# Kernel optimization log

Measured on AMD Instinct MI355X. Metric: run time of the kernel, lower is better.

The kernel has to match this reference:

```python
import jax, jax.numpy as jnp
import numpy as np

IN_CH = 32
H = W = 512
NUM_CAMS = 4096
N_RAYS = 524288
HIDDEN = 128
ALPHA = 1e-4
# tensor_config = ['xy','xz','yz'] -> axis index pairs into t (x,y,z)
AXES = ((0, 1), (0, 2), (1, 2))


def grid_sample_border(plane, coords):
    """Bilinear grid_sample, padding_mode='border', align_corners=True.
    plane: (C,H,W); coords: (N,2) in [-1,1], coords[:,0]->W axis, coords[:,1]->H axis.
    Returns (N,C)."""
    C, Hh, Ww = plane.shape
    x = (coords[:, 0] + 1.0) * 0.5 * (Ww - 1)
    y = (coords[:, 1] + 1.0) * 0.5 * (Hh - 1)
    x0f = jnp.floor(x)
    y0f = jnp.floor(y)
    wx = (x - x0f)[None, :]
    wy = (y - y0f)[None, :]
    x0 = jnp.clip(x0f.astype(jnp.int32), 0, Ww - 1)
    x1 = jnp.clip(x0f.astype(jnp.int32) + 1, 0, Ww - 1)
    y0 = jnp.clip(y0f.astype(jnp.int32), 0, Hh - 1)
    y1 = jnp.clip(y0f.astype(jnp.int32) + 1, 0, Hh - 1)
    v00 = plane[:, y0, x0]  # (C,N)
    v01 = plane[:, y0, x1]
    v10 = plane[:, y1, x0]
    v11 = plane[:, y1, x1]
    out = (v00 * (1 - wx) * (1 - wy) + v01 * wx * (1 - wy)
           + v10 * (1 - wx) * wy + v11 * wx * wy)
    return out.T


def exp_so3(r):
    """Rodrigues: axis-angle (N,3) -> rotation matrices (N,3,3)."""
    theta = jnp.linalg.norm(r, axis=-1)[:, None, None]
    z = jnp.zeros_like(r[:, 0])
    K = jnp.stack([z, -r[:, 2], r[:, 1],
                   r[:, 2], z, -r[:, 0],
                   -r[:, 1], r[:, 0], z], axis=-1).reshape(-1, 3, 3)
    A = jnp.sin(theta) / (theta + 1e-10)
    B = (1.0 - jnp.cos(theta)) / (theta * theta + 1e-10)
    return jnp.eye(3, dtype=r.dtype) + A * K + B * (K @ K)


def setup_inputs() -> dict:
    key = jax.random.key(0)
    ks = jax.random.split(key, 12)
    cam_id = jax.random.randint(ks[0], (N_RAYS,), 0, NUM_CAMS, dtype=jnp.int32)
    t = jax.random.uniform(ks[1], (NUM_CAMS, 3), minval=-1.0, maxval=1.0, dtype=jnp.float32)
    plane_xy = jax.random.normal(ks[2], (IN_CH, H, W), dtype=jnp.float32)
    plane_xz = jax.random.normal(ks[3], (IN_CH, H, W), dtype=jnp.float32)
    plane_yz = jax.random.normal(ks[4], (IN_CH, H, W), dtype=jnp.float32)
    in_chs = IN_CH * 3
    # kaiming_normal_ init: std = sqrt(2/fan_in)
    w1 = jax.random.normal(ks[5], (in_chs, HIDDEN), dtype=jnp.float32) * np.sqrt(2.0 / in_chs)
    b1 = jax.random.normal(ks[6], (HIDDEN,), dtype=jnp.float32) * 0.01
    w2 = jax.random.normal(ks[7], (HIDDEN, HIDDEN), dtype=jnp.float32) * np.sqrt(2.0 / HIDDEN)
    b2 = jax.random.normal(ks[8], (HIDDEN,), dtype=jnp.float32) * 0.01
    w3 = jax.random.normal(ks[9], (HIDDEN, 3), dtype=jnp.float32) * np.sqrt(2.0 / HIDDEN)
    b3 = jax.random.normal(ks[10], (3,), dtype=jnp.float32) * 0.01
    top = jax.random.normal(ks[11], (NUM_CAMS, 3, 4), dtype=jnp.float32)
    bottom = jnp.tile(jnp.array([[[0.0, 0.0, 0.0, 1.0]]], dtype=jnp.float32), (NUM_CAMS, 1, 1))
    init_c2w = jnp.concatenate([top, bottom], axis=1)  # (NUM_CAMS,4,4)
    return {"cam_id": cam_id, "t": t, "plane_xy": plane_xy, "plane_xz": plane_xz,
            "plane_yz": plane_yz, "w1": w1, "b1": b1, "w2": w2, "b2": b2,
            "w3": w3, "b3": b3, "init_c2w": init_c2w}


def reference(cam_id, t, plane_xy, plane_xz, plane_yz, w1, b1, w2, b2, w3, b3, init_c2w):
    ts = t[cam_id]  # (N,3) per-ray translation
    coords_all = jax.lax.stop_gradient(ts)  # coords use t.data in the original
    codes = []
    for plane, (ax, ay) in zip((plane_xy, plane_xz, plane_yz), AXES):
        coords = jnp.stack([coords_all[:, ax], coords_all[:, ay]], axis=-1)
        codes.append(grid_sample_border(plane, coords))  # (N,IN_CH)
    codes = jnp.concatenate(codes, axis=-1)  # (N, 3*IN_CH)
    h = jax.nn.silu(codes @ w1 + b1)
    h = jax.nn.silu(h @ w2 + b2)
    rot = (h @ w3 + b3) * ALPHA  # (N,3) axis-angle
    R = exp_so3(rot)  # (N,3,3)
    c2w34 = jnp.concatenate([R, ts[:, :, None]], axis=-1)  # (N,3,4)
    bottom = jnp.broadcast_to(jnp.array([0.0, 0.0, 0.0, 1.0], dtype=c2w34.dtype),
                              (c2w34.shape[0], 1, 4))
    c2ws = jnp.concatenate([c2w34, bottom], axis=1)  # (N,4,4)
    return c2ws @ init_c2w[cam_id]
```

## Files before the change

### kernel.cpp

```cpp
#include <hip/hip_runtime.h>
#include <hip/hip_bf16.h>
#include <math.h>

#define HWDIM 512
#define HIDDEN 128
#define N_RAYS 524288
#define NUM_CAMS 4096
#define ALPHA 1e-4f

typedef __attribute__((ext_vector_type(4))) float f32x4;
typedef __attribute__((ext_vector_type(8))) short bf16x8;

__device__ __forceinline__ unsigned short f2bf(float f) {
    union { float f; unsigned u; } v; v.f = f;
    unsigned r = v.u + 0x7FFFu + ((v.u >> 16) & 1u);
    return (unsigned short)(r >> 16);
}
__device__ __forceinline__ float bf2f(unsigned short s) {
    union { unsigned u; float f; } v; v.u = ((unsigned)s) << 16;
    return v.f;
}

__global__ __launch_bounds__(256) void sample_kernel(
    const float* __restrict__ t,
    const float* __restrict__ pxy,
    const float* __restrict__ pxz,
    const float* __restrict__ pyz,
    unsigned short* __restrict__ codes)
{
    const int g = blockIdx.x * 256 + threadIdx.x;
    const int cam = g / 192;
    const int r = g - cam * 192;
    const int f = r >> 1;
    const int ysel = r & 1;
    const int p = f >> 5;
    const int c = f & 31;

    const float ts0 = t[cam * 3 + 0];
    const float ts1 = t[cam * 3 + 1];
    const float ts2 = t[cam * 3 + 2];

    const float* plane;
    float cx, cy;
    if (p == 0)      { plane = pxy; cx = ts0; cy = ts1; }
    else if (p == 1) { plane = pxz; cx = ts0; cy = ts2; }
    else             { plane = pyz; cx = ts1; cy = ts2; }

    const float x = (cx + 1.0f) * 0.5f * (float)(HWDIM - 1);
    const float y = (cy + 1.0f) * 0.5f * (float)(HWDIM - 1);
    const float x0f = floorf(x);
    const float y0f = floorf(y);
    const float wx = x - x0f;
    const float wy = y - y0f;
    const int x0 = min(max((int)x0f, 0), HWDIM - 1);
    const int x1 = min(max((int)x0f + 1, 0), HWDIM - 1);
    const int y0 = min(max((int)y0f, 0), HWDIM - 1);
    const int y1 = min(max((int)y0f + 1, 0), HWDIM - 1);

    const int yr = ysel ? y1 : y0;
    const float wyv = ysel ? wy : (1.0f - wy);

    const float* base = plane + (size_t)c * (HWDIM * HWDIM) + yr * HWDIM;
    const float v0 = base[x0];
    const float v1 = base[x1];

    const float row = (v0 * (1.0f - wx) + v1 * wx) * wyv;
    const float other = __shfl_xor(row, 1);
    if (!ysel) codes[cam * 96 + f] = f2bf(row + other);
}

#define W1S 104
#define W2S 136
#define HS  136

__global__ __launch_bounds__(256) void mlp_kernel(
    const unsigned short* __restrict__ codes,
    const float* __restrict__ t,
    const float* __restrict__ w1, const float* __restrict__ b1,
    const float* __restrict__ w2, const float* __restrict__ b2,
    const float* __restrict__ w3, const float* __restrict__ b3,
    const float* __restrict__ init_c2w,
    float* __restrict__ table)
{
    const int tid  = threadIdx.x;
    const int lane = tid & 63;
    const int wave = tid >> 6;
    const int cam0 = blockIdx.x * 16;
    const int ncol = lane & 15;
    const int kgrp = lane >> 4;

    __shared__ unsigned short w1t[128][W1S];
    __shared__ unsigned short w2t[128][W2S];
    __shared__ unsigned short h1t[16][HS];
    __shared__ unsigned short h2t[16][HS];
    __shared__ float b1s[128], b2s[128], w3s[384];
    __shared__ float rotc[16][3];
    __shared__ float c2ws[16][12];

    {
        const float4* w1v = (const float4*)w1;
        for (int i = tid; i < (96 * 128) / 4; i += 256) {
            const float4 v = w1v[i];
            const int flat = i * 4;
            const int k = flat >> 7, n = flat & 127;
            w1t[n + 0][k] = f2bf(v.x);
            w1t[n + 1][k] = f2bf(v.y);
            w1t[n + 2][k] = f2bf(v.z);
            w1t[n + 3][k] = f2bf(v.w);
        }
        const float4* w2v = (const float4*)w2;
        for (int i = tid; i < (128 * 128) / 4; i += 256) {
            const float4 v = w2v[i];
            const int flat = i * 4;
            const int k = flat >> 7, n = flat & 127;
            w2t[n + 0][k] = f2bf(v.x);
            w2t[n + 1][k] = f2bf(v.y);
            w2t[n + 2][k] = f2bf(v.z);
            w2t[n + 3][k] = f2bf(v.w);
        }
    }
    if (tid < 128) { b1s[tid] = b1[tid]; b2s[tid] = b2[tid]; }
    for (int i = tid; i < 384; i += 256) w3s[i] = w3[i];
    __syncthreads();

    const int nb0 = wave * 32 + ncol;
    const int nb1 = nb0 + 16;

    f32x4 acc0, acc1;
    {
        const float bv0 = b1s[nb0], bv1 = b1s[nb1];
        acc0 = (f32x4){bv0, bv0, bv0, bv0};
        acc1 = (f32x4){bv1, bv1, bv1, bv1};
    }
    const unsigned short* arow = codes + (size_t)(cam0 + ncol) * 96;
    #pragma unroll
    for (int k0 = 0; k0 < 96; k0 += 32) {
        const bf16x8 a   = *reinterpret_cast<const bf16x8*>(arow + k0 + kgrp * 8);
        const bf16x8 bb0 = *reinterpret_cast<const bf16x8*>(&w1t[nb0][k0 + kgrp * 8]);
        const bf16x8 bb1 = *reinterpret_cast<const bf16x8*>(&w1t[nb1][k0 + kgrp * 8]);
        acc0 = __builtin_amdgcn_mfma_f32_16x16x32_bf16(a, bb0, acc0, 0, 0, 0);
        acc1 = __builtin_amdgcn_mfma_f32_16x16x32_bf16(a, bb1, acc1, 0, 0, 0);
    }
    #pragma unroll
    for (int r = 0; r < 4; ++r) {
        const int camr = kgrp * 4 + r;
        const float v0 = acc0[r];
        const float v1 = acc1[r];
        h1t[camr][nb0] = f2bf(v0 / (1.0f + __expf(-v0)));
        h1t[camr][nb1] = f2bf(v1 / (1.0f + __expf(-v1)));
    }
    __syncthreads();

    {
        const float bv0 = b2s[nb0], bv1 = b2s[nb1];
        acc0 = (f32x4){bv0, bv0, bv0, bv0};
        acc1 = (f32x4){bv1, bv1, bv1, bv1};
    }
    #pragma unroll
    for (int k0 = 0; k0 < 128; k0 += 32) {
        const bf16x8 a   = *reinterpret_cast<const bf16x8*>(&h1t[ncol][k0 + kgrp * 8]);
        const bf16x8 bb0 = *reinterpret_cast<const bf16x8*>(&w2t[nb0][k0 + kgrp * 8]);
        const bf16x8 bb1 = *reinterpret_cast<const bf16x8*>(&w2t[nb1][k0 + kgrp * 8]);
        acc0 = __builtin_amdgcn_mfma_f32_16x16x32_bf16(a, bb0, acc0, 0, 0, 0);
        acc1 = __builtin_amdgcn_mfma_f32_16x16x32_bf16(a, bb1, acc1, 0, 0, 0);
    }
    #pragma unroll
    for (int r = 0; r < 4; ++r) {
        const int camr = kgrp * 4 + r;
        const float v0 = acc0[r];
        const float v1 = acc1[r];
        h2t[camr][nb0] = f2bf(v0 / (1.0f + __expf(-v0)));
        h2t[camr][nb1] = f2bf(v1 / (1.0f + __expf(-v1)));
    }
    __syncthreads();

    if (tid < 64) {
        const int cam = tid >> 2, c = tid & 3;
        if (c < 3) {
            float acc = b3[c];
            for (int k = 0; k < 128; ++k)
                acc += bf2f(h2t[cam][k]) * w3s[k * 3 + c];
            rotc[cam][c] = acc * ALPHA;
        }
    }
    __syncthreads();

    if (tid < 16) {
        const int cam = tid;
        const float a = rotc[cam][0], b = rotc[cam][1], c = rotc[cam][2];
        const float th2 = a * a + b * b + c * c;
        const float th = sqrtf(th2);
        const float A = sinf(th) / (th + 1e-10f);
        const float B = (1.0f - cosf(th)) / (th2 + 1e-10f);
        const float ts0 = t[(cam0 + cam) * 3 + 0];
        const float ts1 = t[(cam0 + cam) * 3 + 1];
        const float ts2 = t[(cam0 + cam) * 3 + 2];
        c2ws[cam][0]  = 1.0f + B * (-(c * c + b * b));
        c2ws[cam][1]  = A * (-c) + B * (a * b);
        c2ws[cam][2]  = A * b + B * (a * c);
        c2ws[cam][3]  = ts0;
        c2ws[cam][4]  = A * c + B * (a * b);
        c2ws[cam][5]  = 1.0f + B * (-(c * c + a * a));
        c2ws[cam][6]  = A * (-a) + B * (b * c);
        c2ws[cam][7]  = ts1;
        c2ws[cam][8]  = A * (-b) + B * (a * c);
        c2ws[cam][9]  = A * a + B * (b * c);
        c2ws[cam][10] = 1.0f + B * (-(a * a + b * b));
        c2ws[cam][11] = ts2;
    }
    __syncthreads();

    {
        const int cam = tid >> 4, e = tid & 15, i = e >> 2, j = e & 3;
        const float* ic = init_c2w + (size_t)(cam0 + cam) * 16;
        float v;
        if (i < 3) {
            const float* cw = c2ws[cam];
            v = cw[i * 4 + 0] * ic[0 + j]
              + cw[i * 4 + 1] * ic[4 + j]
              + cw[i * 4 + 2] * ic[8 + j]
              + cw[i * 4 + 3] * ic[12 + j];
        } else {
            v = ic[12 + j];
        }
        table[(size_t)cam0 * 16 + tid] = v;
    }
}

__global__ __launch_bounds__(256) void gather_kernel(
    const int* __restrict__ cam_id,
    const float4* __restrict__ table,
    float4* __restrict__ out)
{
    const int idx = blockIdx.x * blockDim.x + threadIdx.x;
    if (idx >= N_RAYS * 4) return;
    const int ray = idx >> 2;
    const int q = idx & 3;
    const int cid = cam_id[ray];
    out[idx] = table[cid * 4 + q];
}

extern "C" void kernel_launch(void* const* d_in, const int* in_sizes, int n_in,
                              void* d_out, int out_size, void* d_ws, size_t ws_size,
                              hipStream_t stream) {
    const int*   cam_id   = (const int*)  d_in[0];
    const float* t        = (const float*)d_in[1];
    const float* pxy      = (const float*)d_in[2];
    const float* pxz      = (const float*)d_in[3];
    const float* pyz      = (const float*)d_in[4];
    const float* w1       = (const float*)d_in[5];
    const float* b1       = (const float*)d_in[6];
    const float* w2       = (const float*)d_in[7];
    const float* b2       = (const float*)d_in[8];
    const float* w3       = (const float*)d_in[9];
    const float* b3       = (const float*)d_in[10];
    const float* init_c2w = (const float*)d_in[11];

    float* table = (float*)d_ws;
    unsigned short* codes = (unsigned short*)((char*)d_ws + NUM_CAMS * 16 * 4);

    sample_kernel<<<(NUM_CAMS * 192) / 256, 256, 0, stream>>>(t, pxy, pxz, pyz, codes);

    mlp_kernel<<<NUM_CAMS / 16, 256, 0, stream>>>(
        codes, t, w1, b1, w2, b2, w3, b3, init_c2w, table);

    const int total = N_RAYS * 4;
    gather_kernel<<<(total + 255) / 256, 256, 0, stream>>>(
        cam_id, (const float4*)table, (float4*)d_out);
}
```

Baseline: 43.76 us.

## Bin cameras by plane row and sample rows cooperatively from LDS

Replaces the per-camera scattered bilinear gathers with a three-stage pipeline. Cameras are first binned by (plane, row) with atomics, then one block per row stages all 32 channels of that row into LDS as bf16, and each block serves the bilinear taps for every camera in its bin. The MLP kernel now sums the two row partials and packs them into an LDS A-tile. This swaps random gathers for coalesced row streaming, but every block reads a full row whether or not any camera falls in it, so each call streams all three planes. It also adds two extra launches, rounds plane values to bf16 before interpolation, and silently drops cameras if a bin exceeds BINCAP.

```diff
diff --git a/kernel.cpp b/kernel.cpp
--- a/kernel.cpp
+++ b/kernel.cpp
@@ -7,6 +7,7 @@
 #define N_RAYS 524288
 #define NUM_CAMS 4096
 #define ALPHA 1e-4f
+#define BINCAP 64
 
 typedef __attribute__((ext_vector_type(4))) float f32x4;
 typedef __attribute__((ext_vector_type(8))) short bf16x8;
@@ -21,52 +22,104 @@
     return v.f;
 }
 
-__global__ __launch_bounds__(256) void sample_kernel(
+__global__ __launch_bounds__(256) void zero_kernel(unsigned int* __restrict__ cnt) {
+    const int i = blockIdx.x * 256 + threadIdx.x;
+    if (i < 3 * HWDIM) cnt[i] = 0u;
+}
+
+__global__ __launch_bounds__(256) void bin_build(
     const float* __restrict__ t,
+    unsigned int* __restrict__ cnt,
+    uint4* __restrict__ bins)
+{
+    const int cam = blockIdx.x * 256 + threadIdx.x;
+    const float ts0 = t[cam * 3 + 0];
+    const float ts1 = t[cam * 3 + 1];
+    const float ts2 = t[cam * 3 + 2];
+
+    #pragma unroll
+    for (int p = 0; p < 3; ++p) {
+        const float cx = (p == 2) ? ts1 : ts0;
+        const float cy = (p == 0) ? ts1 : ts2;
+        const float x = (cx + 1.0f) * 0.5f * (float)(HWDIM - 1);
+        const float y = (cy + 1.0f) * 0.5f * (float)(HWDIM - 1);
+        const float x0f = floorf(x);
+        const float y0f = floorf(y);
+        const float wx = x - x0f;
+        const float wy = y - y0f;
+        const int x0 = min(max((int)x0f, 0), HWDIM - 1);
+        const int x1 = min(max((int)x0f + 1, 0), HWDIM - 1);
+        const int y0 = min(max((int)y0f, 0), HWDIM - 1);
+        const int y1 = min(max((int)y0f + 1, 0), HWDIM - 1);
+
+        #pragma unroll
+        for (int ysel = 0; ysel < 2; ++ysel) {
+            const int row = ysel ? y1 : y0;
+            const float wv = ysel ? wy : (1.0f - wy);
+            const int bin = p * HWDIM + row;
+            const unsigned slot = atomicAdd(&cnt[bin], 1u);
+            if (slot < BINCAP) {
+                uint4 e;
+                e.x = (unsigned)cam | ((unsigned)ysel << 12)
+                    | ((unsigned)x0 << 13) | ((unsigned)x1 << 22);
+                e.y = __float_as_uint(wx);
+                e.z = __float_as_uint(wv);
+                e.w = 0u;
+                bins[bin * BINCAP + slot] = e;
+            }
+        }
+    }
+}
+
+__global__ __launch_bounds__(256) void row_sample(
     const float* __restrict__ pxy,
     const float* __restrict__ pxz,
     const float* __restrict__ pyz,
-    unsigned short* __restrict__ codes)
+    const unsigned int* __restrict__ cnt,
+    const uint4* __restrict__ bins,
+    float* __restrict__ part)
 {
-    const int g = blockIdx.x * 256 + threadIdx.x;
-    const int cam = g / 192;
-    const int r = g - cam * 192;
-    const int f = r >> 1;
-    const int ysel = r & 1;
-    const int p = f >> 5;
-    const int c = f & 31;
-
-    const float ts0 = t[cam * 3 + 0];
-    const float ts1 = t[cam * 3 + 1];
-    const float ts2 = t[cam * 3 + 2];
-
-    const float* plane;
-    float cx, cy;
-    if (p == 0)      { plane = pxy; cx = ts0; cy = ts1; }
-    else if (p == 1) { plane = pxz; cx = ts0; cy = ts2; }
-    else             { plane = pyz; cx = ts1; cy = ts2; }
-
-    const float x = (cx + 1.0f) * 0.5f * (float)(HWDIM - 1);
-    const float y = (cy + 1.0f) * 0.5f * (float)(HWDIM - 1);
-    const float x0f = floorf(x);
-    const float y0f = floorf(y);
-    const float wx = x - x0f;
-    const float wy = y - y0f;
-    const int x0 = min(max((int)x0f, 0), HWDIM - 1);
-    const int x1 = min(max((int)x0f + 1, 0), HWDIM - 1);
-    const int y0 = min(max((int)y0f, 0), HWDIM - 1);
-    const int y1 = min(max((int)y0f + 1, 0), HWDIM - 1);
-
-    const int yr = ysel ? y1 : y0;
-    const float wyv = ysel ? wy : (1.0f - wy);
-
-    const float* base = plane + (size_t)c * (HWDIM * HWDIM) + yr * HWDIM;
-    const float v0 = base[x0];
-    const float v1 = base[x1];
-
-    const float row = (v0 * (1.0f - wx) + v1 * wx) * wyv;
-    const float other = __shfl_xor(row, 1);
-    if (!ysel) codes[cam * 96 + f] = f2bf(row + other);
+    const int p = blockIdx.x >> 9;
+    const int row = blockIdx.x & (HWDIM - 1);
+    const float* plane = (p == 0) ? pxy : ((p == 1) ? pxz : pyz);
+
+    __shared__ unsigned short rowlds[32][514];
+
+    #pragma unroll
+    for (int k = 0; k < 16; ++k) {
+        const int idx = threadIdx.x + 256 * k;
+        const int c = idx >> 7;
+        const int pos = idx & 127;
+        const float4 v = *reinterpret_cast<const float4*>(
+            plane + (size_t)c * (HWDIM * HWDIM) + row * HWDIM + pos * 4);
+        short4 s;
+        s.x = (short)f2bf(v.x);
+        s.y = (short)f2bf(v.y);
+        s.z = (short)f2bf(v.z);
+        s.w = (short)f2bf(v.w);
+        *reinterpret_cast<short4*>(&rowlds[c][pos * 4]) = s;
+    }
+    __syncthreads();
+
+    const int n = min((int)cnt[p * HWDIM + row], BINCAP);
+    const uint4* bb = bins + (size_t)(p * HWDIM + row) * BINCAP;
+
+    for (int j = 0; j < 8; ++j) {
+        const int tau = threadIdx.x + 256 * j;
+        if (tau >= n * 32) break;
+        const int e = tau >> 5;
+        const int c = tau & 31;
+        const uint4 E = bb[e];
+        const int cam  = (int)(E.x & 4095u);
+        const int ysel = (int)((E.x >> 12) & 1u);
+        const int x0   = (int)((E.x >> 13) & 511u);
+        const int x1   = (int)((E.x >> 22) & 511u);
+        const float wx = __uint_as_float(E.y);
+        const float wv = __uint_as_float(E.z);
+        const float v0 = bf2f(rowlds[c][x0]);
+        const float v1 = bf2f(rowlds[c][x1]);
+        part[(size_t)cam * 192 + p * 64 + ysel * 32 + c] = (v0 + (v1 - v0) * wx) * wv;
+    }
 }
 
 #define W1S 104
@@ -74,7 +127,7 @@
 #define HS  136
 
 __global__ __launch_bounds__(256) void mlp_kernel(
-    const unsigned short* __restrict__ codes,
+    const float* __restrict__ part,
     const float* __restrict__ t,
     const float* __restrict__ w1, const float* __restrict__ b1,
     const float* __restrict__ w2, const float* __restrict__ b2,
@@ -91,6 +144,7 @@
 
     __shared__ unsigned short w1t[128][W1S];
     __shared__ unsigned short w2t[128][W2S];
+    __shared__ unsigned short h0t[16][W1S];
     __shared__ unsigned short h1t[16][HS];
     __shared__ unsigned short h2t[16][HS];
     __shared__ float b1s[128], b2s[128], w3s[384];
@@ -119,6 +173,14 @@
             w2t[n + 3][k] = f2bf(v.w);
         }
     }
+    #pragma unroll
+    for (int j = 0; j < 6; ++j) {
+        const int idx = tid + 256 * j;
+        const int cl = idx / 96;
+        const int f = idx - cl * 96;
+        const size_t base = (size_t)(cam0 + cl) * 192 + (f >> 5) * 64 + (f & 31);
+        h0t[cl][f] = f2bf(part[base] + part[base + 32]);
+    }
     if (tid < 128) { b1s[tid] = b1[tid]; b2s[tid] = b2[tid]; }
     for (int i = tid; i < 384; i += 256) w3s[i] = w3[i];
     __syncthreads();
@@ -132,10 +194,9 @@
         acc0 = (f32x4){bv0, bv0, bv0, bv0};
         acc1 = (f32x4){bv1, bv1, bv1, bv1};
     }
-    const unsigned short* arow = codes + (size_t)(cam0 + ncol) * 96;
     #pragma unroll
     for (int k0 = 0; k0 < 96; k0 += 32) {
-        const bf16x8 a   = *reinterpret_cast<const bf16x8*>(arow + k0 + kgrp * 8);
+        const bf16x8 a   = *reinterpret_cast<const bf16x8*>(&h0t[ncol][k0 + kgrp * 8]);
         const bf16x8 bb0 = *reinterpret_cast<const bf16x8*>(&w1t[nb0][k0 + kgrp * 8]);
         const bf16x8 bb1 = *reinterpret_cast<const bf16x8*>(&w1t[nb1][k0 + kgrp * 8]);
         acc0 = __builtin_amdgcn_mfma_f32_16x16x32_bf16(a, bb0, acc0, 0, 0, 0);
@@ -256,14 +317,17 @@
     const float* b3       = (const float*)d_in[10];
     const float* init_c2w = (const float*)d_in[11];
 
-    float* table = (float*)d_ws;
-    unsigned short* codes = (unsigned short*)((char*)d_ws + NUM_CAMS * 16 * 4);
-
-    sample_kernel<<<(NUM_CAMS * 192) / 256, 256, 0, stream>>>(t, pxy, pxz, pyz, codes);
-
+    char* ws = (char*)d_ws;
+    float* table = (float*)ws;
+    float* part  = (float*)(ws + 262144);
+    unsigned int* cnt = (unsigned int*)(ws + 262144 + 3145728);
+    uint4* bins = (uint4*)(ws + 262144 + 3145728 + 6144);
+
+    zero_kernel<<<6, 256, 0, stream>>>(cnt);
+    bin_build<<<NUM_CAMS / 256, 256, 0, stream>>>(t, cnt, bins);
+    row_sample<<<3 * HWDIM, 256, 0, stream>>>(pxy, pxz, pyz, cnt, bins, part);
     mlp_kernel<<<NUM_CAMS / 16, 256, 0, stream>>>(
-        codes, t, w1, b1, w2, b2, w3, b3, init_c2w, table);
-
+        part, t, w1, b1, w2, b2, w3, b3, init_c2w, table);
     const int total = N_RAYS * 4;
     gather_kernel<<<(total + 255) / 256, 256, 0, stream>>>(
         cam_id, (const float4*)table, (float4*)d_out);
```

Result: slower. 55.96 us (+27.9%).
